# Optimization experiments

Measured on AMD Instinct MI355X. Metric: run time of the kernel, lower is better.

Reference implementation:

```python
import jax, jax.numpy as jnp
import numpy as np

B_COEF = 0.1          # position-offset scale 'b'
STRIDE = (1, 1)
PADDING = (1, 1)


def setup_inputs() -> dict:
    key = jax.random.key(0)
    k1, k2, k3 = jax.random.split(key, 3)
    x = jax.random.normal(k1, (16, 64, 128, 128), dtype=jnp.float32)
    kernel = jax.random.normal(k2, (128, 64, 3, 3), dtype=jnp.float32)
    bias = jax.random.normal(k3, (128,), dtype=jnp.float32)
    return {"x": x, "kernel": kernel, "bias": bias}


def _conv(inp, w):
    pads = [(PADDING[0], PADDING[0]), (PADDING[1], PADDING[1])]
    return jax.lax.conv_general_dilated(
        inp, w, window_strides=STRIDE, padding=pads,
        dimension_numbers=("NCHW", "OIHW", "NCHW"))


def reference(x, kernel, bias):
    # out[b,o,p] = sum_i x_unf[b,i,p] * (kernel_flat[o,i] + b*grid[p]) + bias[o]
    # = conv(x, kernel) + b*grid[p] * sum_i x_unf[b,i,p] + bias  (rank-1 separable)
    kh, kw = kernel.shape[2], kernel.shape[3]
    main = _conv(x, kernel)                                  # (B, O, Ho, Wo)
    H_out, W_out = main.shape[2], main.shape[3]

    # sum over in_channels and kernel window = ones-conv of channel-summed input
    ones_k = jnp.ones((1, 1, kh, kw), dtype=x.dtype)
    patch_sum = _conv(x.sum(axis=1, keepdims=True), ones_k)  # (B, 1, Ho, Wo)

    # Replicate torch meshgrid(arange(W_out), arange(H_out), indexing='ij')
    # -> flatten (W,H) row-major -> consumed as (H,W) row-major by the view.
    gx = jnp.arange(W_out)[:, None] + jnp.arange(H_out)[None, :]  # (Wo, Ho)
    grid2d = gx.reshape(-1).reshape(H_out, W_out).astype(x.dtype)  # (Ho, Wo)

    return main + B_COEF * grid2d * patch_sum + bias[None, :, None, None]
```

## Files before the change

### kernel.cpp

```cpp
#include <hip/hip_runtime.h>
#include <hip/hip_bf16.h>


typedef __attribute__((ext_vector_type(8))) short short8;
typedef __attribute__((ext_vector_type(4))) float f32x4;

#define B_COEF 0.1f
constexpr int CI = 64, CO = 128, H = 128, W = 128;
constexpr int XPAD = 72;

static __device__ inline short bf16s(float v) {
    __hip_bfloat16 b = __float2bfloat16(v);
    return *reinterpret_cast<short*>(&b);
}


__global__ __launch_bounds__(256)
void prep_x(const float* __restrict__ x, __hip_bfloat16* __restrict__ xt,
            float* __restrict__ S) {
    __shared__ float tile[64 * 132];
    __shared__ float psum[8 * 128];
    const int bx = blockIdx.x, b = blockIdx.y, tid = threadIdx.x;
    const int h = ((bx & 7) << 4) | (bx >> 3);
    const int q = tid & 31, cbase = tid >> 5;

    const float* xp = x + (((size_t)b * CI + cbase * 8) * H + h) * W + q * 4;
    f32x4 v[8];
#pragma unroll
    for (int it = 0; it < 8; ++it)
        v[it] = *(const f32x4*)(xp + (size_t)it * H * W);

    const int cw = 4 * (q ^ cbase);
    f32x4 sacc = v[0];
#pragma unroll
    for (int it = 0; it < 8; ++it) {
        *(f32x4*)&tile[(cbase * 8 + it) * 132 + cw] = v[it];
        if (it) sacc += v[it];
    }
    *(f32x4*)&psum[cbase * 128 + 4 * q] = sacc;
    __syncthreads();

    if (tid < 128) {
        float s = 0.0f;
#pragma unroll
        for (int g = 0; g < 8; ++g) s += psum[g * 128 + tid];
        S[((size_t)b * H + h) * W + tid] = s;
    }

    const int c8 = (tid & 7) * 8, wl = tid >> 3, sw = 4 * (tid & 7);
#pragma unroll
    for (int it = 0; it < 4; ++it) {
        int ww = wl + it * 32;
        short8 pk;
#pragma unroll
        for (int j = 0; j < 8; ++j)
            pk[j] = bf16s(tile[(c8 + j) * 132 + (ww ^ sw)]);
        *(short8*)(xt + (((size_t)b * H + h) * W + ww) * CI + c8) = pk;
    }
}

__global__ void prep_wq(const float* __restrict__ wgt, __hip_bfloat16* __restrict__ wq) {
    int idx = blockIdx.x * 256 + threadIdx.x;
    if (idx < 9 * CO * CI) {
        int tap = idx >> 13;
        int rem = idx & 8191;
        int oc = rem >> 6, ci = rem & 63;
        int kc = ci >> 5, j = ci & 31;
        wq[(((tap * 2 + kc) * CO + oc) << 5) + j] =
            __float2bfloat16(wgt[(oc * CI + ci) * 9 + tap]);
    }
}

__global__ __launch_bounds__(256, 4)
void conv_main(const __hip_bfloat16* __restrict__ xt,
               const __hip_bfloat16* __restrict__ wq,
               const float* __restrict__ S,
               const float* __restrict__ bias,
               float* __restrict__ out) {
    __shared__ __hip_bfloat16 xrow[3][66 * XPAD];
    __shared__ float ssum[68];

    const int tid = threadIdx.x, bx = blockIdx.x, b = blockIdx.y;
    const int u = ((bx & 7) << 5) | (bx >> 3);
    const int h = u >> 1, w0 = (u & 1) * 64;
    const int lane = tid & 63, waveid = tid >> 6;
    const int lo16 = lane & 15, quad = lane >> 4;
    const int n0 = waveid * 32;

    const int c8 = (tid & 7) * 8, wl = tid >> 3;
#pragma unroll
    for (int r = 0; r < 3; ++r) {
        const int gh = h - 1 + r;
#pragma unroll
        for (int it = 0; it < 3; ++it) {
            int w = wl + it * 32;
            if (w < 66) {
                int gw = w0 + w - 1;
                short8 v = {0, 0, 0, 0, 0, 0, 0, 0};
                if (gh >= 0 && gh < H && gw >= 0 && gw < W)
                    v = *(const short8*)(xt + (((size_t)b * H + gh) * W + gw) * CI + c8);
                *(short8*)&xrow[r][w * XPAD + c8] = v;
            }
        }
    }
    if (tid < 66) {
        int gw = w0 + tid - 1;
        float s = 0.0f;
        if (gw >= 0 && gw < W) {
#pragma unroll
            for (int r = 0; r < 3; ++r) {
                int gh = h - 1 + r;
                if (gh >= 0 && gh < H) s += S[((size_t)b * H + gh) * W + gw];
            }
        }
        ssum[tid] = s;
    }
    __syncthreads();

    f32x4 acc[4][2] = {};

#pragma unroll
    for (int kh = 0; kh < 3; ++kh) {
#pragma unroll
        for (int kw = 0; kw < 3; ++kw) {
            const int tap = kh * 3 + kw;
            short8 bq[2][2];
#pragma unroll
            for (int kc = 0; kc < 2; ++kc)
#pragma unroll
                for (int ni = 0; ni < 2; ++ni)
                    bq[kc][ni] = *(const short8*)(
                        wq + (((tap * 2 + kc) * CO + n0 + ni * 16 + lo16) << 5) + quad * 8);
#pragma unroll
            for (int kc = 0; kc < 2; ++kc) {
                short8 af[4];
#pragma unroll
                for (int mi = 0; mi < 4; ++mi)
                    af[mi] = *(const short8*)
                        &xrow[kh][(mi * 16 + lo16 + kw) * XPAD + kc * 32 + quad * 8];
#pragma unroll
                for (int mi = 0; mi < 4; ++mi)
#pragma unroll
                    for (int ni = 0; ni < 2; ++ni)
                        acc[mi][ni] = __builtin_amdgcn_mfma_f32_16x16x32_bf16(
                            af[mi], bq[kc][ni], acc[mi][ni], 0, 0, 0);
            }
        }
    }

#pragma unroll
    for (int mi = 0; mi < 4; ++mi) {
        const int wbase = mi * 16 + quad * 4;
        float cs[6];
#pragma unroll
        for (int t = 0; t < 6; ++t) cs[t] = ssum[wbase + t];
        float ps[4], cf[4];
#pragma unroll
        for (int t = 0; t < 4; ++t) {
            ps[t] = cs[t] + cs[t + 1] + cs[t + 2];
            cf[t] = B_COEF * (float)(h + w0 + wbase + t);
        }
#pragma unroll
        for (int ni = 0; ni < 2; ++ni) {
            const int oc = n0 + ni * 16 + lo16;
            const float bv = bias[oc];
            f32x4 v = acc[mi][ni];
#pragma unroll
            for (int t = 0; t < 4; ++t) v[t] = v[t] + cf[t] * ps[t] + bv;
            *(f32x4*)(out + (((size_t)b * CO + oc) * H + h) * W + w0 + wbase) = v;
        }
    }
}


constexpr int WPAD = 72;

__global__ void prep_w_fb(const float* __restrict__ wgt, __hip_bfloat16* __restrict__ wt) {
    int idx = blockIdx.x * 256 + threadIdx.x;
    if (idx < 9 * CO * CI) {
        int tap = idx / (CO * CI);
        int rem = idx - tap * (CO * CI);
        int oc = rem >> 6, ci = rem & 63;
        wt[idx] = __float2bfloat16(wgt[(oc * CI + ci) * 9 + tap]);
    }
}

__global__ __launch_bounds__(256, 2)
void conv_fb(const float* __restrict__ x, const __hip_bfloat16* __restrict__ wt,
             const float* __restrict__ bias, float* __restrict__ out) {
    __shared__ __hip_bfloat16 xrow[130 * XPAD];
    __shared__ __hip_bfloat16 wlds[CO * WPAD];
    __shared__ float colsum[132];

    const int tid = threadIdx.x;
    const int h = blockIdx.x, b = blockIdx.y;
    const int lane = tid & 63, waveid = tid >> 6;
    const int lo16 = lane & 15, quad = lane >> 4;
    const int m0 = (waveid & 1) * 64, n0 = (waveid >> 1) * 64;

    f32x4 acc[4][4] = {};
    if (tid < 132) colsum[tid] = 0.0f;
    const float* xb = x + (size_t)b * CI * H * W;

    const int w16 = tid & 15, cipl = (tid >> 4) & 3, rest0 = tid >> 6;

    for (int kh = 0; kh < 3; ++kh) {
        const int gh = h - 1 + kh;
        __syncthreads();
        for (int it = 0; it < 18; ++it) {
            int rest = rest0 + it * 4;
            int whi = rest % 9, ciph = rest / 9;
            int w = whi * 16 + w16;
            int ci0 = (ciph * 4 + cipl) * 2;
            int gw = w - 1;
            float x0 = 0.0f, x1 = 0.0f;
            if (w < 130 && gw >= 0 && gw < W && gh >= 0 && gh < H) {
                const float* p = xb + (size_t)ci0 * (H * W) + gh * W + gw;
                x0 = p[0];
                x1 = p[H * W];
            }
            if (w < 130) {
                __hip_bfloat162 pk;
                pk.x = __float2bfloat16(x0);
                pk.y = __float2bfloat16(x1);
                *(__hip_bfloat162*)&xrow[w * XPAD + ci0] = pk;
            }
            float cs = x0 + x1;
            cs += __shfl_xor(cs, 16);
            cs += __shfl_xor(cs, 32);
            if (quad == 0 && w < 130) atomicAdd(&colsum[w], cs);
        }
        for (int kw = 0; kw < 3; ++kw) {
            __syncthreads();
            {
                const __hip_bfloat16* wtap = wt + (kh * 3 + kw) * (CO * CI);
#pragma unroll
                for (int it = 0; it < 4; ++it) {
                    int j = tid + it * 256;
                    int oc = j >> 3, ch = (j & 7) * 8;
                    short8 v = *(const short8*)(wtap + oc * CI + ch);
                    *(short8*)&wlds[oc * WPAD + ch] = v;
                }
            }
            __syncthreads();
#pragma unroll
            for (int kc = 0; kc < 2; ++kc) {
                const int krow = kc * 32 + quad * 8;
                short8 af[4], bf[4];
#pragma unroll
                for (int mi = 0; mi < 4; ++mi)
                    af[mi] = *(const short8*)&xrow[(m0 + mi * 16 + lo16 + kw) * XPAD + krow];
#pragma unroll
                for (int ni = 0; ni < 4; ++ni)
                    bf[ni] = *(const short8*)&wlds[(n0 + ni * 16 + lo16) * WPAD + krow];
#pragma unroll
                for (int mi = 0; mi < 4; ++mi)
#pragma unroll
                    for (int ni = 0; ni < 4; ++ni)
                        acc[mi][ni] = __builtin_amdgcn_mfma_f32_16x16x32_bf16(
                            af[mi], bf[ni], acc[mi][ni], 0, 0, 0);
            }
        }
    }
    __syncthreads();
#pragma unroll
    for (int mi = 0; mi < 4; ++mi) {
        const int wbase = m0 + mi * 16 + quad * 4;
        float cs[6];
#pragma unroll
        for (int r = 0; r < 6; ++r) cs[r] = colsum[wbase + r];
        float ps[4], cf[4];
#pragma unroll
        for (int r = 0; r < 4; ++r) {
            ps[r] = cs[r] + cs[r + 1] + cs[r + 2];
            cf[r] = B_COEF * (float)(h + wbase + r);
        }
#pragma unroll
        for (int ni = 0; ni < 4; ++ni) {
            const int oc = n0 + ni * 16 + lo16;
            const float bv = bias[oc];
            f32x4 v = acc[mi][ni];
#pragma unroll
            for (int r = 0; r < 4; ++r) v[r] = v[r] + cf[r] * ps[r] + bv;
            *(f32x4*)(out + (((size_t)b * CO + oc) * H + h) * W + wbase) = v;
        }
    }
}


extern "C" void kernel_launch(void* const* d_in, const int* in_sizes, int n_in,
                              void* d_out, int out_size, void* d_ws, size_t ws_size,
                              hipStream_t stream) {
    const float* x    = (const float*)d_in[0];
    const float* wgt  = (const float*)d_in[1];
    const float* bias = (const float*)d_in[2];
    float* out = (float*)d_out;

    const size_t XT_BYTES = (size_t)16 * H * W * CI * 2;
    const size_t S_BYTES  = (size_t)16 * H * W * 4;
    const size_t WQ_BYTES = (size_t)9 * 2 * CO * 32 * 2;

    if (ws_size >= XT_BYTES + S_BYTES + WQ_BYTES) {
        __hip_bfloat16* xt = (__hip_bfloat16*)d_ws;
        float* S           = (float*)((char*)d_ws + XT_BYTES);
        __hip_bfloat16* wq = (__hip_bfloat16*)((char*)d_ws + XT_BYTES + S_BYTES);
        prep_x<<<dim3(H, 16), dim3(256), 0, stream>>>(x, xt, S);
        prep_wq<<<dim3(288), dim3(256), 0, stream>>>(wgt, wq);
        conv_main<<<dim3(2 * H, 16), dim3(256), 0, stream>>>(xt, wq, S, bias, out);
    } else {
        __hip_bfloat16* wt = (__hip_bfloat16*)d_ws;
        prep_w_fb<<<dim3(288), dim3(256), 0, stream>>>(wgt, wt);
        conv_fb<<<dim3(H, 16), dim3(256), 0, stream>>>(x, wt, bias, out);
    }
}
```

Measured before the change: 238.9 us.

## Load conv input rows via global_load_lds with XOR swizzle, fuse weight prep

The conv kernel now fills its input-row tile in LDS with direct global-to-LDS 16-byte loads and an XOR-swizzled layout instead of padded rows. Out-of-bounds rows read from a zero page appended to the weight buffer. Weight conversion moves into extra blocks of prep_x, removing one launch. MFMA section runs at raised wave priority. The aim is to cut register round-trips, bank conflicts and launch overhead, at the cost of more complex addressing and reliance on the zero page.

```diff
diff --git a/kernel.cpp b/kernel.cpp
--- a/kernel.cpp
+++ b/kernel.cpp
@@ -14,13 +14,36 @@
     return *reinterpret_cast<short*>(&b);
 }
 
+static __device__ inline void gload16(const void* g, const void* l) {
+    __builtin_amdgcn_global_load_lds(
+        (const __attribute__((address_space(1))) void*)g,
+        (__attribute__((address_space(3))) void*)l, 16, 0, 0);
+}
+
 
 __global__ __launch_bounds__(256)
-void prep_x(const float* __restrict__ x, __hip_bfloat16* __restrict__ xt,
-            float* __restrict__ S) {
+void prep_x(const float* __restrict__ x, const float* __restrict__ wgt,
+            __hip_bfloat16* __restrict__ xt, float* __restrict__ S,
+            __hip_bfloat16* __restrict__ wq) {
     __shared__ float tile[64 * 132];
     __shared__ float psum[8 * 128];
     const int bx = blockIdx.x, b = blockIdx.y, tid = threadIdx.x;
+
+    if (bx >= H) {
+        int t = ((bx - H) * 16 + b) * 256 + tid;
+        int oc = t >> 6, ci = t & 63;
+        int kc = ci >> 5, j = ci & 31;
+#pragma unroll
+        for (int tap = 0; tap < 9; ++tap)
+            wq[(((tap * 2 + kc) * CO + oc) << 5) + j] =
+                __float2bfloat16(wgt[(oc * CI + ci) * 9 + tap]);
+        if (t == 0) {
+            short8 z = {0, 0, 0, 0, 0, 0, 0, 0};
+            *(short8*)(wq + 9 * 2 * CO * 32) = z;
+        }
+        return;
+    }
+
     const int h = ((bx & 7) << 4) | (bx >> 3);
     const int q = tid & 31, cbase = tid >> 5;
 
@@ -56,18 +79,6 @@
         for (int j = 0; j < 8; ++j)
             pk[j] = bf16s(tile[(c8 + j) * 132 + (ww ^ sw)]);
         *(short8*)(xt + (((size_t)b * H + h) * W + ww) * CI + c8) = pk;
-    }
-}
-
-__global__ void prep_wq(const float* __restrict__ wgt, __hip_bfloat16* __restrict__ wq) {
-    int idx = blockIdx.x * 256 + threadIdx.x;
-    if (idx < 9 * CO * CI) {
-        int tap = idx >> 13;
-        int rem = idx & 8191;
-        int oc = rem >> 6, ci = rem & 63;
-        int kc = ci >> 5, j = ci & 31;
-        wq[(((tap * 2 + kc) * CO + oc) << 5) + j] =
-            __float2bfloat16(wgt[(oc * CI + ci) * 9 + tap]);
     }
 }
 
@@ -77,7 +88,7 @@
                const float* __restrict__ S,
                const float* __restrict__ bias,
                float* __restrict__ out) {
-    __shared__ __hip_bfloat16 xrow[3][66 * XPAD];
+    __shared__ __hip_bfloat16 xrow[3][72 * 64];
     __shared__ float ssum[68];
 
     const int tid = threadIdx.x, bx = blockIdx.x, b = blockIdx.y;
@@ -87,22 +98,25 @@
     const int lo16 = lane & 15, quad = lane >> 4;
     const int n0 = waveid * 32;
 
-    const int c8 = (tid & 7) * 8, wl = tid >> 3;
-#pragma unroll
-    for (int r = 0; r < 3; ++r) {
+    const __hip_bfloat16* zpage = wq + 9 * 2 * CO * 32;
+
+    const int wl = lane >> 3;
+    const int ul = (lane & 7) ^ wl;
+    const int lane_elem = wl * 64 + ul * 8;
+    for (int idx = waveid; idx < 27; idx += 4) {
+        const int r = idx / 9, seg = idx - r * 9;
+        const int wb = seg * 8;
         const int gh = h - 1 + r;
-#pragma unroll
-        for (int it = 0; it < 3; ++it) {
-            int w = wl + it * 32;
-            if (w < 66) {
-                int gw = w0 + w - 1;
-                short8 v = {0, 0, 0, 0, 0, 0, 0, 0};
-                if (gh >= 0 && gh < H && gw >= 0 && gw < W)
-                    v = *(const short8*)(xt + (((size_t)b * H + gh) * W + gw) * CI + c8);
-                *(short8*)&xrow[r][w * XPAD + c8] = v;
-            }
-        }
-    }
+        const int wlds = wb + wl;
+        const int gw = w0 + wlds - 1;
+        const bool valid =
+            (gh >= 0) && (gh < H) && (gw >= 0) && (gw < W) && (wlds < 66);
+        const void* src = valid
+            ? (const void*)(xt + (((size_t)b * H + gh) * W + w0 + wb - 1) * CI + lane_elem)
+            : (const void*)zpage;
+        gload16(src, &xrow[r][wb * 64]);
+    }
+
     if (tid < 66) {
         int gw = w0 + tid - 1;
         float s = 0.0f;
@@ -119,6 +133,7 @@
 
     f32x4 acc[4][2] = {};
 
+    __builtin_amdgcn_s_setprio(1);
 #pragma unroll
     for (int kh = 0; kh < 3; ++kh) {
 #pragma unroll
@@ -135,9 +150,11 @@
             for (int kc = 0; kc < 2; ++kc) {
                 short8 af[4];
 #pragma unroll
-                for (int mi = 0; mi < 4; ++mi)
+                for (int mi = 0; mi < 4; ++mi) {
+                    const int row = mi * 16 + lo16 + kw;
                     af[mi] = *(const short8*)
-                        &xrow[kh][(mi * 16 + lo16 + kw) * XPAD + kc * 32 + quad * 8];
+                        &xrow[kh][row * 64 + (((kc * 4 + quad) ^ (row & 7)) * 8)];
+                }
 #pragma unroll
                 for (int mi = 0; mi < 4; ++mi)
 #pragma unroll
@@ -147,6 +164,7 @@
             }
         }
     }
+    __builtin_amdgcn_s_setprio(0);
 
 #pragma unroll
     for (int mi = 0; mi < 4; ++mi) {
@@ -298,14 +316,13 @@
 
     const size_t XT_BYTES = (size_t)16 * H * W * CI * 2;
     const size_t S_BYTES  = (size_t)16 * H * W * 4;
-    const size_t WQ_BYTES = (size_t)9 * 2 * CO * 32 * 2;
+    const size_t WQ_BYTES = (size_t)9 * 2 * CO * 32 * 2 + 64;
 
     if (ws_size >= XT_BYTES + S_BYTES + WQ_BYTES) {
         __hip_bfloat16* xt = (__hip_bfloat16*)d_ws;
         float* S           = (float*)((char*)d_ws + XT_BYTES);
         __hip_bfloat16* wq = (__hip_bfloat16*)((char*)d_ws + XT_BYTES + S_BYTES);
-        prep_x<<<dim3(H, 16), dim3(256), 0, stream>>>(x, xt, S);
-        prep_wq<<<dim3(288), dim3(256), 0, stream>>>(wgt, wq);
+        prep_x<<<dim3(H + 2, 16), dim3(256), 0, stream>>>(x, wgt, xt, S, wq);
         conv_main<<<dim3(2 * H, 16), dim3(256), 0, stream>>>(xt, wq, S, bias, out);
     } else {
         __hip_bfloat16* wt = (__hip_bfloat16*)d_ws;
```

Result: faster. 231.1 us (-3.2%).
